# Kernel optimization log

Measured on AMD Instinct MI355X. Metric: run time of the kernel, lower is better.

## Reference

```python
import jax, jax.numpy as jnp
import numpy as np

W = 8            # fine window (sqrt of feat_0's WW)
WP2 = W + 2      # feat_1 search window side (10)
SLICE = 8
TEMP = 10.0


def setup_inputs() -> dict:
    key = jax.random.key(0)
    ks = jax.random.split(key, 6)
    M = 8192
    C = 64
    return {
        'feat_0': jax.random.normal(ks[0], (M, W * W, C), dtype=jnp.float32),
        'feat_1': jax.random.normal(ks[1], (M, WP2 * WP2, C), dtype=jnp.float32),
        'mkpts0_c': jax.random.uniform(ks[2], (M, 2), dtype=jnp.float32) * 800.0,
        'mkpts1_c': jax.random.uniform(ks[3], (M, 2), dtype=jnp.float32) * 800.0,
        'mconf': jax.random.uniform(ks[4], (M,), dtype=jnp.float32),
        'b_ids': jnp.zeros((M,), dtype=jnp.int64),
        'hw0_i': 832,
        'hw0_f': 416,
        'bs': 1,
    }


def reference(feat_0, feat_1, mkpts0_c, mkpts1_c, mconf, b_ids, hw0_i, hw0_f, bs):
    M, WW, C = feat_0.shape                      # WW = W*W = 64
    scale = float(hw0_i) / float(hw0_f)          # image -> fine-feature stride

    feat_f0, feat_ff0 = feat_0[..., :-SLICE], feat_0[..., -SLICE:]
    feat_f1, feat_ff1 = feat_1[..., :-SLICE], feat_1[..., -SLICE:]

    # note: BOTH sides divided by sqrt(C) in the source -> overall 1/C
    conf_f = jnp.einsum('mlc,mrc->mlr', feat_f0, feat_f1) * (1.0 / C)          # [M,64,100]
    conf_ff = jnp.einsum('mlc,mrc->mlr', feat_ff0, feat_ff1) / np.sqrt(SLICE)  # [M,64,100]

    # dual softmax, then crop the 10x10 search window to the inner 8x8
    sm = jax.nn.softmax(conf_f, axis=1) * jax.nn.softmax(conf_f, axis=2)
    sm = sm.reshape(M, WW, WP2, WP2)[..., 1:-1, 1:-1].reshape(M, WW, WW)       # [M,64,64]

    # ---- get_fine_ds_match (torch.no_grad in source) ----
    flat = jax.lax.stop_gradient(sm.reshape(M, WW * WW))
    idx = jnp.argmax(flat, axis=-1)                # [M]
    idx_l, idx_r = idx // WW, idx % WW             # each in [0,64)
    gy, gx = jnp.meshgrid(jnp.arange(W), jnp.arange(W), indexing='ij')
    grid = (jnp.stack([gx, gy], -1).reshape(WW, 2).astype(feat_0.dtype)
            - (W // 2) + 0.5)                      # (x,y) pixel offsets, centered
    delta_l = grid[idx_l]                          # [M,2]
    delta_r = grid[idx_r]
    mkpts0_f = jax.lax.stop_gradient(mkpts0_c) + delta_l * scale
    mkpts1_mid = jax.lax.stop_gradient(mkpts1_c) + delta_r * scale

    # ---- 3x3 window gather in the (W+2)x(W+2) map (faithful index arithmetic) ----
    iids, jids = idx_r // W, idx_r % W             # [0,8)
    d = jnp.arange(3) - 1                          # {-1,0,1}
    wi = iids[:, None, None] + d[None, :, None]    # [M,3,3] rows, may be -1
    wj = jids[:, None, None] + d[None, None, :]    # [M,3,3] cols
    wi = jnp.where(wi < 0, wi + WP2, wi)           # torch negative-index wrap
    wj = jnp.where(wj < 0, wj + WP2, wj)
    cff = conf_ff.reshape(M, WW, WP2, WP2)
    win = cff[jnp.arange(M)[:, None, None], idx_l[:, None, None], wi, wj]  # [M,3,3]

    probs = jax.nn.softmax(win.reshape(M, 9) / TEMP, axis=-1)              # [M,9]
    heat = probs.reshape(M, 3, 3)
    pos = jnp.linspace(-1.0, 1.0, 3).astype(feat_0.dtype)
    coord_x = jnp.sum(heat * pos[None, None, :], axis=(1, 2))              # over width
    coord_y = jnp.sum(heat * pos[None, :, None], axis=(1, 2))              # over height
    coords = jnp.stack([coord_x, coord_y], -1)     # [M,2] soft-argmax, (x,y)

    scale1 = scale                                 # bs == 1 branch
    mkpts1_f = mkpts1_mid + coords * (3 // 2) * scale1
    return (mkpts0_f, mkpts1_f, probs, sm)
```

## Files before the change

### kernel.cpp

```cpp
#include <hip/hip_runtime.h>
#include <math.h>
#include <limits.h>


constexpr int TPB = 256;

typedef _Float16 half8_t __attribute__((ext_vector_type(8)));
typedef _Float16 half4_t __attribute__((ext_vector_type(4)));
typedef float    float4_t __attribute__((ext_vector_type(4)));

struct __align__(16) SMem {
    union {
        struct {
            unsigned short f1h[100 * 56];
            unsigned short f1l[100 * 56];
        };
        float sm[64 * 64];
    };
    unsigned short f0h[64 * 56];
    unsigned short f0l[64 * 56];
    float ff0[64 * 8];
    float ff1[100 * 8];
    float cpart[4][112];
    float csum[112];
    float wval[4];
    int   widx[4];
    float win[9];
};

__global__ __launch_bounds__(TPB, 3) void fine_matching_kernel(
    const float* __restrict__ feat0,
    const float* __restrict__ feat1,
    const float* __restrict__ mk0,
    const float* __restrict__ mk1,
    const int* __restrict__ hw0_i,
    const int* __restrict__ hw0_f,
    float* __restrict__ out, int M)
{
    __shared__ SMem S;

    const int m = blockIdx.x;
    const int t = threadIdx.x;
    const int lane = t & 63;
    const int w = t >> 6;
    const int col = lane & 15;
    const int q = lane >> 4;
    const float scale = (float)hw0_i[0] / (float)hw0_f[0];

    const float* g0 = feat0 + (size_t)m * 4096;
    const float* g1 = feat1 + (size_t)m * 6400;
    _Float16* f0h = (_Float16*)S.f0h;
    _Float16* f0l = (_Float16*)S.f0l;
    _Float16* f1h = (_Float16*)S.f1h;
    _Float16* f1l = (_Float16*)S.f1l;

    for (int i = t; i < 1024; i += TPB) {
        float4_t v = ((const float4_t*)g0)[i];
        int fl = i << 2, l = fl >> 6, c = fl & 63;
        if (c < 56) {
            half4_t hi, lo;
            #pragma unroll
            for (int j = 0; j < 4; j++) {
                float x = v[j];
                _Float16 h = (_Float16)x;
                hi[j] = h;
                lo[j] = (_Float16)(x - (float)h);
            }
            *(half4_t*)(f0h + l * 56 + c) = hi;
            *(half4_t*)(f0l + l * 56 + c) = lo;
        } else {
            *(float4_t*)&S.ff0[l * 8 + (c - 56)] = v;
        }
    }
    for (int i = t; i < 1600; i += TPB) {
        float4_t v = ((const float4_t*)g1)[i];
        int fl = i << 2, l = fl >> 6, c = fl & 63;
        if (c < 56) {
            half4_t hi, lo;
            #pragma unroll
            for (int j = 0; j < 4; j++) {
                float x = v[j];
                _Float16 h = (_Float16)x;
                hi[j] = h;
                lo[j] = (_Float16)(x - (float)h);
            }
            *(half4_t*)(f1h + l * 56 + c) = hi;
            *(half4_t*)(f1l + l * 56 + c) = lo;
        } else {
            *(float4_t*)&S.ff1[l * 8 + (c - 56)] = v;
        }
    }
    __syncthreads();

    float4_t acc[7];
    #pragma unroll
    for (int rt = 0; rt < 7; rt++)
        #pragma unroll
        for (int j = 0; j < 4; j++) acc[rt][j] = 0.0f;

    half8_t hz;
    #pragma unroll
    for (int j = 0; j < 8; j++) hz[j] = (_Float16)0.0f;

    const int arow = (16 * w + col) * 56;
    #pragma unroll
    for (int ks = 0; ks < 2; ks++) {
        int koff = ks ? (32 + q * 8) : (q * 8);
        const bool kz = (ks == 1) && (q == 3);
        if (kz) koff = 0;
        half8_t ah = *(const half8_t*)(f0h + arow + koff);
        half8_t al = *(const half8_t*)(f0l + arow + koff);
        if (kz) { ah = hz; al = hz; }
        #pragma unroll
        for (int rt = 0; rt < 7; rt++) {
            int brow = rt * 16 + col;
            if (brow > 99) brow = 99;
            const int bo = brow * 56 + koff;
            half8_t bh = *(const half8_t*)(f1h + bo);
            half8_t bl = *(const half8_t*)(f1l + bo);
            acc[rt] = __builtin_amdgcn_mfma_f32_16x16x32_f16(ah, bh, acc[rt], 0, 0, 0);
            acc[rt] = __builtin_amdgcn_mfma_f32_16x16x32_f16(al, bh, acc[rt], 0, 0, 0);
            acc[rt] = __builtin_amdgcn_mfma_f32_16x16x32_f16(ah, bl, acc[rt], 0, 0, 0);
        }
    }

    float p[7][4];
    #pragma unroll
    for (int rt = 0; rt < 7; rt++) {
        const bool rvalid = (rt < 6) || (col < 4);
        #pragma unroll
        for (int j = 0; j < 4; j++) {
            float c = acc[rt][j] * (1.0f / 64.0f);
            p[rt][j] = rvalid ? __expf(c) : 0.0f;
        }
    }

    float invr[4];
    #pragma unroll
    for (int j = 0; j < 4; j++) {
        float s = 0.0f;
        #pragma unroll
        for (int rt = 0; rt < 7; rt++) s += p[rt][j];
        s += __shfl_xor(s, 1); s += __shfl_xor(s, 2);
        s += __shfl_xor(s, 4); s += __shfl_xor(s, 8);
        invr[j] = 1.0f / s;
    }

    #pragma unroll
    for (int rt = 0; rt < 7; rt++) {
        float s = p[rt][0] + p[rt][1] + p[rt][2] + p[rt][3];
        s += __shfl_xor(s, 16);
        s += __shfl_xor(s, 32);
        if (lane < 16) S.cpart[w][rt * 16 + col] = s;
    }
    __syncthreads();
    if (t < 112)
        S.csum[t] = S.cpart[0][t] + S.cpart[1][t] + S.cpart[2][t] + S.cpart[3][t];
    __syncthreads();

    float invc[7];
    #pragma unroll
    for (int rt = 0; rt < 7; rt++) {
        const bool rvalid = (rt < 6) || (col < 4);
        invc[rt] = rvalid ? 1.0f / S.csum[rt * 16 + col] : 0.0f;
    }

    float* s_sm = S.sm;
    float bestv = -INFINITY; int besti = INT_MAX;
    #pragma unroll
    for (int j = 0; j < 4; j++) {
        const int l = 16 * w + 4 * q + j;
        #pragma unroll
        for (int rt = 0; rt < 7; rt++) {
            const int r = rt * 16 + col;
            if (r < 100) {
                const int ri = r / 10, rj = r - ri * 10;
                if (ri >= 1 && ri <= 8 && rj >= 1 && rj <= 8) {
                    float pv = p[rt][j];
                    float v = pv * pv * invr[j] * invc[rt];
                    int flat = l * 64 + (ri - 1) * 8 + (rj - 1);
                    s_sm[flat] = v;
                    if (v > bestv) { bestv = v; besti = flat; }
                }
            }
        }
    }
    #pragma unroll
    for (int d = 1; d < 64; d <<= 1) {
        float ov = __shfl_xor(bestv, d);
        int   oi = __shfl_xor(besti, d);
        if (ov > bestv || (ov == bestv && oi < besti)) { bestv = ov; besti = oi; }
    }
    if (lane == 0) { S.wval[w] = bestv; S.widx[w] = besti; }
    __syncthreads();

    float bv = S.wval[0]; int best = S.widx[0];
    #pragma unroll
    for (int i = 1; i < 4; i++) {
        float v2 = S.wval[i]; int i2 = S.widx[i];
        if (v2 > bv || (v2 == bv && i2 < best)) { bv = v2; best = i2; }
    }
    const int idx_l = best >> 6;
    const int idx_r = best & 63;
    const int iids  = idx_r >> 3, jids = idx_r & 7;

    float* o_sm = out + (size_t)13 * M + (size_t)m * 4096;
    for (int i = t; i < 1024; i += TPB)
        ((float4_t*)o_sm)[i] = ((const float4_t*)s_sm)[i];

    if (t < 9) {
        int da = t / 3 - 1, db = t % 3 - 1;
        int wi = iids + da; if (wi < 0) wi += 10;
        int wj = jids + db; if (wj < 0) wj += 10;
        int rp = wi * 10 + wj;
        float dot = 0.0f;
        #pragma unroll
        for (int c = 0; c < 8; c++)
            dot += S.ff0[idx_l * 8 + c] * S.ff1[rp * 8 + c];
        S.win[t] = dot * 0.35355339059327373f;
    }
    __syncthreads();

    if (t == 0) {
        float ww[9], mx = -INFINITY;
        #pragma unroll
        for (int i = 0; i < 9; i++) { ww[i] = S.win[i] * 0.1f; mx = fmaxf(mx, ww[i]); }
        float sum = 0.0f;
        #pragma unroll
        for (int i = 0; i < 9; i++) { ww[i] = __expf(ww[i] - mx); sum += ww[i]; }
        float inv = 1.0f / sum;
        float* o_probs = out + (size_t)4 * M + (size_t)m * 9;
        float cx = 0.0f, cy = 0.0f;
        #pragma unroll
        for (int i = 0; i < 9; i++) {
            float pb = ww[i] * inv;
            o_probs[i] = pb;
            cx += pb * (float)(i % 3 - 1);
            cy += pb * (float)(i / 3 - 1);
        }
        float dlx = (float)(idx_l & 7) - 3.5f;
        float dly = (float)(idx_l >> 3) - 3.5f;
        out[2 * m]     = mk0[2 * m]     + dlx * scale;
        out[2 * m + 1] = mk0[2 * m + 1] + dly * scale;
        float drx = (float)jids - 3.5f;
        float dry = (float)iids - 3.5f;
        float* o1 = out + (size_t)2 * M;
        o1[2 * m]     = mk1[2 * m]     + (drx + cx) * scale;
        o1[2 * m + 1] = mk1[2 * m + 1] + (dry + cy) * scale;
    }
}

extern "C" void kernel_launch(void* const* d_in, const int* in_sizes, int n_in,
                              void* d_out, int out_size, void* d_ws, size_t ws_size,
                              hipStream_t stream) {
    const float* feat0 = (const float*)d_in[0];
    const float* feat1 = (const float*)d_in[1];
    const float* mk0   = (const float*)d_in[2];
    const float* mk1   = (const float*)d_in[3];
    const int*   hw0_i = (const int*)d_in[6];
    const int*   hw0_f = (const int*)d_in[7];
    const int M = in_sizes[0] / 4096;

    fine_matching_kernel<<<M, TPB, 0, stream>>>(
        feat0, feat1, mk0, mk1, hw0_i, hw0_f, (float*)d_out, M);
}
```

Before: 455.0 us.

## Load feat_0 A fragments directly into registers and drop feat_0 shared staging

Each lane now reads its feat_0 A-operand fragment straight from global memory into registers and splits it into fp16 hi/lo there, so the f0h/f0l shared arrays go away. The ff0/ff1 regression channels are no longer staged either; the 9-thread window dot product re-reads those 8 floats from global. The smaller shared footprint lets occupancy rise, and launch bounds are raised from 3 to 6 blocks per CU. The costs are uncoalesced per-lane global reads for A, a few extra global loads in the tail, and tighter register limits at the higher occupancy target.

Measured after the change: 421.8 us. 7.3% less time.

```diff
diff --git a/kernel.cpp b/kernel.cpp
--- a/kernel.cpp
+++ b/kernel.cpp
@@ -17,10 +17,6 @@
         };
         float sm[64 * 64];
     };
-    unsigned short f0h[64 * 56];
-    unsigned short f0l[64 * 56];
-    float ff0[64 * 8];
-    float ff1[100 * 8];
     float cpart[4][112];
     float csum[112];
     float wval[4];
@@ -28,7 +24,7 @@
     float win[9];
 };
 
-__global__ __launch_bounds__(TPB, 3) void fine_matching_kernel(
+__global__ __launch_bounds__(TPB, 6) void fine_matching_kernel(
     const float* __restrict__ feat0,
     const float* __restrict__ feat1,
     const float* __restrict__ mk0,
@@ -49,47 +45,51 @@
 
     const float* g0 = feat0 + (size_t)m * 4096;
     const float* g1 = feat1 + (size_t)m * 6400;
-    _Float16* f0h = (_Float16*)S.f0h;
-    _Float16* f0l = (_Float16*)S.f0l;
     _Float16* f1h = (_Float16*)S.f1h;
     _Float16* f1l = (_Float16*)S.f1l;
 
-    for (int i = t; i < 1024; i += TPB) {
-        float4_t v = ((const float4_t*)g0)[i];
-        int fl = i << 2, l = fl >> 6, c = fl & 63;
-        if (c < 56) {
-            half4_t hi, lo;
-            #pragma unroll
-            for (int j = 0; j < 4; j++) {
-                float x = v[j];
-                _Float16 h = (_Float16)x;
-                hi[j] = h;
-                lo[j] = (_Float16)(x - (float)h);
-            }
-            *(half4_t*)(f0h + l * 56 + c) = hi;
-            *(half4_t*)(f0l + l * 56 + c) = lo;
-        } else {
-            *(float4_t*)&S.ff0[l * 8 + (c - 56)] = v;
-        }
-    }
+    const int arow = (16 * w + col) * 64;
+    float4_t araw[2][2];
+    #pragma unroll
+    for (int ks = 0; ks < 2; ks++) {
+        const int koff = ks ? (32 + q * 8) : (q * 8);
+        araw[ks][0] = *(const float4_t*)(g0 + arow + koff);
+        araw[ks][1] = *(const float4_t*)(g0 + arow + koff + 4);
+    }
+
     for (int i = t; i < 1600; i += TPB) {
+        const int fl = i << 2, l = fl >> 6, c = fl & 63;
+        if (c >= 56) continue;
         float4_t v = ((const float4_t*)g1)[i];
-        int fl = i << 2, l = fl >> 6, c = fl & 63;
-        if (c < 56) {
-            half4_t hi, lo;
-            #pragma unroll
-            for (int j = 0; j < 4; j++) {
-                float x = v[j];
-                _Float16 h = (_Float16)x;
-                hi[j] = h;
-                lo[j] = (_Float16)(x - (float)h);
-            }
-            *(half4_t*)(f1h + l * 56 + c) = hi;
-            *(half4_t*)(f1l + l * 56 + c) = lo;
-        } else {
-            *(float4_t*)&S.ff1[l * 8 + (c - 56)] = v;
-        }
-    }
+        half4_t hi, lo;
+        #pragma unroll
+        for (int j = 0; j < 4; j++) {
+            float x = v[j];
+            _Float16 h = (_Float16)x;
+            hi[j] = h;
+            lo[j] = (_Float16)(x - (float)h);
+        }
+        *(half4_t*)(f1h + l * 56 + c) = hi;
+        *(half4_t*)(f1l + l * 56 + c) = lo;
+    }
+
+    half8_t hz;
+    #pragma unroll
+    for (int j = 0; j < 8; j++) hz[j] = (_Float16)0.0f;
+
+    half8_t ah[2], al[2];
+    #pragma unroll
+    for (int ks = 0; ks < 2; ks++) {
+        #pragma unroll
+        for (int j = 0; j < 8; j++) {
+            float x = araw[ks][j >> 2][j & 3];
+            _Float16 h = (_Float16)x;
+            ah[ks][j] = h;
+            al[ks][j] = (_Float16)(x - (float)h);
+        }
+    }
+    if (q == 3) { ah[1] = hz; al[1] = hz; }
+
     __syncthreads();
 
     float4_t acc[7];
@@ -98,29 +98,21 @@
         #pragma unroll
         for (int j = 0; j < 4; j++) acc[rt][j] = 0.0f;
 
-    half8_t hz;
-    #pragma unroll
-    for (int j = 0; j < 8; j++) hz[j] = (_Float16)0.0f;
-
-    const int arow = (16 * w + col) * 56;
     #pragma unroll
     for (int ks = 0; ks < 2; ks++) {
-        int koff = ks ? (32 + q * 8) : (q * 8);
+        const int koff = ks ? (32 + q * 8) : (q * 8);
         const bool kz = (ks == 1) && (q == 3);
-        if (kz) koff = 0;
-        half8_t ah = *(const half8_t*)(f0h + arow + koff);
-        half8_t al = *(const half8_t*)(f0l + arow + koff);
-        if (kz) { ah = hz; al = hz; }
+        const int bkoff = kz ? 0 : koff;
         #pragma unroll
         for (int rt = 0; rt < 7; rt++) {
             int brow = rt * 16 + col;
             if (brow > 99) brow = 99;
-            const int bo = brow * 56 + koff;
+            const int bo = brow * 56 + bkoff;
             half8_t bh = *(const half8_t*)(f1h + bo);
             half8_t bl = *(const half8_t*)(f1l + bo);
-            acc[rt] = __builtin_amdgcn_mfma_f32_16x16x32_f16(ah, bh, acc[rt], 0, 0, 0);
-            acc[rt] = __builtin_amdgcn_mfma_f32_16x16x32_f16(al, bh, acc[rt], 0, 0, 0);
-            acc[rt] = __builtin_amdgcn_mfma_f32_16x16x32_f16(ah, bl, acc[rt], 0, 0, 0);
+            acc[rt] = __builtin_amdgcn_mfma_f32_16x16x32_f16(ah[ks], bh, acc[rt], 0, 0, 0);
+            acc[rt] = __builtin_amdgcn_mfma_f32_16x16x32_f16(al[ks], bh, acc[rt], 0, 0, 0);
+            acc[rt] = __builtin_amdgcn_mfma_f32_16x16x32_f16(ah[ks], bl, acc[rt], 0, 0, 0);
         }
     }
 
@@ -213,10 +205,13 @@
         int wi = iids + da; if (wi < 0) wi += 10;
         int wj = jids + db; if (wj < 0) wj += 10;
         int rp = wi * 10 + wj;
+        float4_t a0 = *(const float4_t*)(g0 + idx_l * 64 + 56);
+        float4_t a1 = *(const float4_t*)(g0 + idx_l * 64 + 60);
+        float4_t b0 = *(const float4_t*)(g1 + rp * 64 + 56);
+        float4_t b1 = *(const float4_t*)(g1 + rp * 64 + 60);
         float dot = 0.0f;
         #pragma unroll
-        for (int c = 0; c < 8; c++)
-            dot += S.ff0[idx_l * 8 + c] * S.ff1[rp * 8 + c];
+        for (int j = 0; j < 4; j++) dot += a0[j] * b0[j] + a1[j] * b1[j];
         S.win[t] = dot * 0.35355339059327373f;
     }
     __syncthreads();
```
